# Kernel tuning notes

Measured on AMD Instinct MI355X. Metric: run time of the kernel, lower is better.

## Reference

```python
import jax, jax.numpy as jnp
import numpy as np

B, N = 16, 80
TEXT_DIM, AUDIO_DIM = 1024, 512
FD, FO = 512, 512          # bilinear pooling D, O
DH = 384                   # hidden_dim
L = 2                      # gnn_layers
NC = 7                     # num_class
IN_DIM = DH * (L + 1) + FO # out_mlp input dim


def _w(key, shape, scale=0.02):
    return (jax.random.normal(key, shape, dtype=jnp.float32) * scale)


def setup_inputs() -> dict:
    key = jax.random.key(0)
    ks = list(jax.random.split(key, 40))
    inp = {
        "features_text": jax.random.normal(ks[0], (B, N, TEXT_DIM), dtype=jnp.float32),
        "features_audio": jax.random.normal(ks[1], (B, N, AUDIO_DIM), dtype=jnp.float32),
        "adj": jnp.ones((B, N, N), dtype=jnp.int32),
        "s_mask": jax.random.randint(ks[2], (B, N, N), 0, 2, dtype=jnp.int32),
        "s_mask_onehot": jnp.zeros((B, N, N, 2), dtype=jnp.float32),
        "lengths": jnp.full((N and B,), N, dtype=jnp.int64) if False else jnp.full((B,), N, dtype=jnp.int32),
        # bilinear pooling
        "U1_w": _w(ks[3], (FD, TEXT_DIM)),
        "U2_w": _w(ks[4], (FD, AUDIO_DIM)),
        "P_w": _w(ks[5], (FO, FD)), "P_b": jnp.zeros((FO,), jnp.float32),
        "V1_w": _w(ks[6], (FO, TEXT_DIM)),
        "V2_w": _w(ks[7], (FO, AUDIO_DIM)),
        # fc1
        "fc1_w": _w(ks[8], (DH, FO)), "fc1_b": jnp.zeros((DH,), jnp.float32),
        # per-layer GAT (stacked on leading layer dim)
        "gat_w": _w(ks[9], (L, 1, 2 * DH)), "gat_b": jnp.zeros((L, 1), jnp.float32),
        "Wr0": _w(ks[10], (L, DH, DH)), "Wr1": _w(ks[11], (L, DH, DH)),
        # GRU cells (torch GRUCell layout: weight_ih (3H,H), weight_hh (3H,H))
        "gruC_wi": _w(ks[12], (L, 3 * DH, DH)), "gruC_wh": _w(ks[13], (L, 3 * DH, DH)),
        "gruC_bi": jnp.zeros((L, 3 * DH), jnp.float32), "gruC_bh": jnp.zeros((L, 3 * DH), jnp.float32),
        "gruP_wi": _w(ks[14], (L, 3 * DH, DH)), "gruP_wh": _w(ks[15], (L, 3 * DH, DH)),
        "gruP_bi": jnp.zeros((L, 3 * DH), jnp.float32), "gruP_bh": jnp.zeros((L, 3 * DH), jnp.float32),
        # out_mlp: Linear(in_dim,H) ReLU, Linear(H,H) ReLU, Linear(H,NC)
        "mlp_w0": _w(ks[16], (DH, IN_DIM)), "mlp_b0": jnp.zeros((DH,), jnp.float32),
        "mlp_w1": _w(ks[17], (DH, DH)), "mlp_b1": jnp.zeros((DH,), jnp.float32),
        "mlp_w2": _w(ks[18], (NC, DH)), "mlp_b2": jnp.zeros((NC,), jnp.float32),
    }
    return inp


def _gru_cell(x, h, wi, wh, bi, bh):
    gi = x @ wi.T + bi
    gh = h @ wh.T + bh
    i_r, i_z, i_n = jnp.split(gi, 3, axis=-1)
    h_r, h_z, h_n = jnp.split(gh, 3, axis=-1)
    r = jax.nn.sigmoid(i_r + h_r)
    z = jax.nn.sigmoid(i_z + h_z)
    n = jnp.tanh(i_n + r * h_n)
    return (1.0 - z) * n + z * h


def reference(features_text, features_audio, adj, s_mask, s_mask_onehot, lengths,
              U1_w, U2_w, P_w, P_b, V1_w, V2_w, fc1_w, fc1_b,
              gat_w, gat_b, Wr0, Wr1,
              gruC_wi, gruC_wh, gruC_bi, gruC_bh,
              gruP_wi, gruP_wh, gruP_bi, gruP_bh,
              mlp_w0, mlp_b0, mlp_w1, mlp_b1, mlp_w2, mlp_b2):
    # bilinear pooling fusion
    c_ = jax.nn.sigmoid(features_text @ U1_w.T) * jax.nn.sigmoid(features_audio @ U2_w.T)
    fused = c_ @ P_w.T + P_b + features_text @ V1_w.T + features_audio @ V2_w.T  # (B,N,FO)
    H0 = jax.nn.relu(fused @ fc1_w.T + fc1_b)                                    # (B,N,DH)

    n = H0.shape[1]
    adj_f = adj.astype(H0.dtype)
    s_f = s_mask.astype(H0.dtype)
    pos = jnp.arange(n)
    adj_t = jnp.swapaxes(adj_f, 0, 1)  # (N,B,N)
    s_t = jnp.swapaxes(s_f, 0, 1)      # (N,B,N)

    Hs = [H0]
    for l in range(gat_w.shape[0]):
        wq, wk = gat_w[l, 0, :H0.shape[2]], gat_w[l, 0, H0.shape[2]:]
        gb = gat_b[l, 0]
        wr0, wr1 = Wr0[l], Wr1[l]
        cwi, cwh, cbi, cbh = gruC_wi[l], gruC_wh[l], gruC_bi[l], gruC_bh[l]
        pwi, pwh, pbi, pbh = gruP_wi[l], gruP_wh[l], gruP_bi[l], gruP_bh[l]
        Hl = Hs[-1]

        def step(H1, xs):
            xi, adj_i, s_i, i = xs                              # xi (B,DH)
            # GAT_dialoggcn_v1 score: linear(cat(Q,K))
            alpha = (xi @ wq)[:, None] + H1 @ wk + gb           # (B,N)
            mask = adj_i * (pos < i).astype(alpha.dtype)        # only past, adj-allowed
            alpha = alpha - (1.0 - mask) * 1e30
            w = jax.nn.softmax(alpha, axis=-1)                  # (B,N)
            sm = s_i[..., None]
            V = (H1 @ wr0.T) * sm + (H1 @ wr1.T) * (1.0 - sm)   # (B,N,DH)
            M = jnp.einsum('bn,bnd->bd', w, V)
            M = jnp.where(i == 0, jnp.zeros_like(M), M)         # i=0: no attention, M=0
            C = _gru_cell(xi, M, cwi, cwh, cbi, cbh)
            P = _gru_cell(M, xi, pwi, pwh, pbi, pbh)
            Hnew = C + P
            H1 = jax.lax.dynamic_update_slice(H1, Hnew[:, None, :], (0, i, 0))
            return H1, Hnew

        xs = (jnp.swapaxes(Hl, 0, 1), adj_t, s_t, jnp.arange(n))
        _, ys = jax.lax.scan(step, jnp.zeros_like(Hl), xs)
        Hs.append(jnp.swapaxes(ys, 0, 1))

    Hcat = jnp.concatenate(Hs + [fused], axis=2)  # (B,N,IN_DIM)
    # attentive_node_features with nodal_att_type=None is identity; dropout eval = identity
    h = jax.nn.relu(Hcat @ mlp_w0.T + mlp_b0)
    h = jax.nn.relu(h @ mlp_w1.T + mlp_b1)
    logits = h @ mlp_w2.T + mlp_b2
    return jax.nn.log_softmax(logits, axis=2)
```

## Files before the change

kernel.cpp:

```cpp
#include <hip/hip_runtime.h>
#include <hip/hip_bf16.h>
#include <math.h>

#define BB 16
#define NN 80
#define DH_ 384
#define LDH 1664

typedef unsigned int uint;
typedef unsigned long long u64;

__global__ __launch_bounds__(256)
void gemm64(const float* __restrict__ A, int lda,
            const float* __restrict__ W, const float* __restrict__ Wb, int ldw,
            const float* __restrict__ bias,
            float* __restrict__ C, int ldc,
            int K, int act, int accum)
{
    __shared__ float As[16][68];
    __shared__ float Bs[16][68];
    const int tid = threadIdx.x;
    const int tx = tid & 15, ty = tid >> 4;
    const int r0 = blockIdx.y * 64, o0 = blockIdx.x * 64;

    float acc[4][4];
#pragma unroll
    for (int u = 0; u < 4; ++u)
#pragma unroll
        for (int v = 0; v < 4; ++v) acc[u][v] = 0.f;

    const int srow = tid >> 2;
    const int kq = (tid & 3) << 2;
    const float* asrc = A + (r0 + srow) * lda;
    const float* wsrc;
    {
        int orow = o0 + srow;
        wsrc = (Wb && orow >= 512) ? (Wb + (orow - 512) * ldw) : (W + orow * ldw);
    }

    for (int kb = 0; kb < K; kb += 16) {
        float4 va = *(const float4*)(asrc + kb + kq);
        float4 vb = *(const float4*)(wsrc + kb + kq);
        As[kq + 0][srow] = va.x; As[kq + 1][srow] = va.y;
        As[kq + 2][srow] = va.z; As[kq + 3][srow] = va.w;
        Bs[kq + 0][srow] = vb.x; Bs[kq + 1][srow] = vb.y;
        Bs[kq + 2][srow] = vb.z; Bs[kq + 3][srow] = vb.w;
        __syncthreads();
#pragma unroll
        for (int k = 0; k < 16; ++k) {
            float4 a = *(const float4*)&As[k][ty * 4];
            float4 bv = *(const float4*)&Bs[k][tx * 4];
            float av[4] = {a.x, a.y, a.z, a.w};
            float bb[4] = {bv.x, bv.y, bv.z, bv.w};
#pragma unroll
            for (int u = 0; u < 4; ++u)
#pragma unroll
                for (int v = 0; v < 4; ++v)
                    acc[u][v] = fmaf(av[u], bb[v], acc[u][v]);
        }
        __syncthreads();
    }
#pragma unroll
    for (int u = 0; u < 4; ++u) {
        int r = r0 + ty * 4 + u;
#pragma unroll
        for (int v = 0; v < 4; ++v) {
            int o = o0 + tx * 4 + v;
            float c = acc[u][v];
            if (bias) c += bias[o];
            if (accum) c += C[r * ldc + o];
            if (act == 1) c = fmaxf(c, 0.f);
            else if (act == 2) c = 1.f / (1.f + expf(-c));
            else if (act == 3 && o < 512) c = 1.f / (1.f + expf(-c));
            C[r * ldc + o] = c;
        }
    }
}

__global__ void ew2(const float* __restrict__ T1, const float* __restrict__ T2,
                    float* __restrict__ CBuf, float* __restrict__ Hc)
{
    int idx = blockIdx.x * 256 + threadIdx.x;
    int r = idx >> 9, c = idx & 511;
    CBuf[idx] = T1[r * 1024 + c] * T2[r * 1024 + c];
    Hc[r * LDH + 1152 + c] = T1[r * 1024 + 512 + c] + T2[r * 1024 + 512 + c];
}

__device__ __forceinline__ uint packbf(float lo, float hi)
{
    uint a = __float_as_uint(lo);
    a = (a + 0x7fffu + ((a >> 16) & 1u)) >> 16;
    uint b = __float_as_uint(hi);
    b = (b + 0x7fffu + ((b >> 16) & 1u)) & 0xffff0000u;
    return a | b;
}
__device__ __forceinline__ float bflo(uint u) { return __uint_as_float(u << 16); }
__device__ __forceinline__ float bfhi(uint u) { return __uint_as_float(u & 0xffff0000u); }

__global__ void trans_wg3(const float* __restrict__ cwh, const float* __restrict__ pwi,
                          uint* __restrict__ WgPk)
{
    int idx = blockIdx.x * 256 + threadIdx.x;
    int l = idx / 442368;
    int r = idx % 442368;
    int g = r / 27648;
    int r2 = r % 27648;
    int k = r2 / 72, cp = r2 % 72;
    float v[2];
#pragma unroll
    for (int u = 0; u < 2; ++u) {
        int c = 2 * cp + u;
        int idx6 = c / 24, o = c % 24, d = g * 24 + o;
        v[u] = (idx6 < 3) ? cwh[l * 442368 + (idx6 * 384 + d) * 384 + k]
                          : pwi[l * 442368 + ((idx6 - 3) * 384 + d) * 384 + k];
    }
    WgPk[idx] = packbf(v[0], v[1]);
}

__global__ void trans_wr3(const float* __restrict__ Wr0, const float* __restrict__ Wr1,
                          uint* __restrict__ WrPk)
{
    int idx = blockIdx.x * 256 + threadIdx.x;
    int l = idx / 147456;
    int r = idx % 147456;
    int g = r / 9216;
    int r2 = r % 9216;
    int k = r2 / 24, dl = r2 % 24;
    int row = g * 24 + dl;
    float w0 = Wr0[l * 147456 + row * 384 + k];
    float w1 = Wr1[l * 147456 + row * 384 + k];
    WrPk[idx] = packbf(w0, w1);
}

__global__ void gpre_prep(const float* __restrict__ cwi, const float* __restrict__ pwh,
                          const float* __restrict__ cbi, const float* __restrict__ pbh,
                          float* __restrict__ gw, float* __restrict__ gb_)
{
    int idx = blockIdx.x * 256 + threadIdx.x;
    int l = idx / 884736;
    int r = idx % 884736;
    int o = r / 384, k = r % 384;
    gw[idx] = (o < 1152) ? cwi[l * 442368 + o * 384 + k]
                         : pwh[l * 442368 + (o - 1152) * 384 + k];
    if (k == 0)
        gb_[l * 2304 + o] = (o < 1152) ? cbi[l * 1152 + o] : pbh[l * 1152 + o - 1152];
}

__global__ __launch_bounds__(256)
void qpre_k(const float* __restrict__ Hc, int hin, const float* __restrict__ wq,
            float* __restrict__ q)
{
    int wave = threadIdx.x >> 6, lane = threadIdx.x & 63;
    int row = blockIdx.x * 4 + wave;
    const float* hp = Hc + row * LDH + hin;
    float s = 0.f;
#pragma unroll
    for (int u = 0; u < 6; ++u) s = fmaf(hp[lane + 64 * u], wq[lane + 64 * u], s);
#pragma unroll
    for (int m = 1; m < 64; m <<= 1) s += __shfl_xor(s, m);
    if (lane == 0) q[row] = s;
}

#define ALD64(p)    __hip_atomic_load((p), __ATOMIC_RELAXED, __HIP_MEMORY_SCOPE_AGENT)
#define AST64(p, v) __hip_atomic_store((p), (v), __ATOMIC_RELAXED, __HIP_MEMORY_SCOPE_AGENT)

__global__ __launch_bounds__(512)
void scan10(float* Hc, int hin, int hout,
            const float* __restrict__ gPre,
            const uint* __restrict__ WrPkl,
            const uint* __restrict__ WgPkl,
            const float* __restrict__ qpre,
            const float* __restrict__ gatwl,
            const float* __restrict__ gatbl,
            const int* __restrict__ adj,
            const int* __restrict__ smask,
            const float* __restrict__ cbh,
            const float* __restrict__ pbi,
            u64* __restrict__ X1,
            u64* __restrict__ X2)
{
    const int wg = blockIdx.x;
    const int b = wg >> 4, g = wg & 15;
    const int t = threadIdx.x;

    extern __shared__ uint WgL[];
    __shared__ uint WrL[384 * 25];
    __shared__ uint Pc16[NN][25];
    __shared__ float kvS[NN];
    __shared__ float2 ws01[NN];
    __shared__ float Mv[DH_];
    __shared__ float uA[864];
    __shared__ float gs[144];
    __shared__ float karr[16];

    {
        const uint* src = WgPkl + g * 27648;
        for (int idx = t; idx < 27648; idx += 512) WgL[idx] = src[idx];
        const uint* src2 = WrPkl + g * 9216;
        for (int idx = t; idx < 9216; idx += 512) {
            int k = idx / 24, dl = idx % 24;
            WrL[k * 25 + dl] = src2[idx];
        }
    }
    __syncthreads();

    u64* X1b = X1 + b * 1024;
    u64* X2b = X2 + b * 512;
    const float gb = gatbl[0];

    int ca0 = 0, cs0 = 0, ca1 = 0, cs1 = 0;
    float cq = 0.f;
    int na0 = 0, ns0 = 0, na1 = 0, ns1 = 0;
    float nq = 0.f;

    float gpv = 0.f, xv = 0.f;

    for (int i = 0; i < NN; ++i) {
        const int rowi = b * NN + i;

        if (t < 144) gpv = gPre[rowi * 2304 + (t / 24) * 384 + g * 24 + (t % 24)];
        else if (t < 168) xv = Hc[rowi * LDH + hin + g * 24 + (t - 144)];
        if (t < 64) {
            int ip = (i + 1 < NN) ? (i + 1) : (NN - 1);
            int rp = b * NN + ip;
            na0 = adj[rp * NN + t];
            ns0 = smask[rp * NN + t];
            if (t + 64 < NN) { na1 = adj[rp * NN + t + 64]; ns1 = smask[rp * NN + t + 64]; }
            nq = qpre[rp];
        }
        __syncthreads();

        if (i > 0) {
            const u64* Xs2 = X2b + ((i - 1) & 1) * 256;
            if (t < 256) {
                int gg = t >> 4, j = t & 15;
                if (j < 13) {
                    u64 w;
                    do { w = ALD64(&Xs2[gg * 16 + j]); } while ((uint)(w >> 32) != (uint)i);
                    uint lo = (uint)w;
                    if (j < 12) {
                        uA[gg * 24 + 2 * j]     = bflo(lo);
                        uA[gg * 24 + 2 * j + 1] = bfhi(lo);
                    } else {
                        karr[gg] = __uint_as_float(lo);
                    }
                }
            }
            __syncthreads();

            if (t == 400) {
                float s = 0.f;
#pragma unroll
                for (int u = 0; u < 16; ++u) s += karr[u];
                kvS[i - 1] = s;
            }
            if (t < 384) {
                int dl0 = t >> 4, sub = t & 15, part = sub & 7, half = sub >> 3;
                float acc = 0.f;
#pragma unroll 8
                for (int m = 0; m < 48; ++m) {
                    int k = part + 8 * m;
                    uint u = WrL[k * 25 + dl0];
                    float w2_ = half ? bfhi(u) : bflo(u);
                    acc = fmaf(w2_, uA[k], acc);
                }
                acc += __shfl_xor(acc, 1);
                acc += __shfl_xor(acc, 2);
                acc += __shfl_xor(acc, 4);
                float other = __shfl_xor(acc, 8);
                if (sub == 0) Pc16[i - 1][dl0] = packbf(acc, other);
            }
            __syncthreads();

            if (t < 64) {
                float q = cq + gb;
                int j0 = t, j1 = t + 64;
                float a0v = -1e30f, a1v = -1e30f;
                if (j0 < i && ca0 != 0) a0v = q + kvS[j0];
                if (j1 < i && ca1 != 0) a1v = q + kvS[j1];
                float mx = fmaxf(a0v, a1v);
#pragma unroll
                for (int m = 1; m < 64; m <<= 1) mx = fmaxf(mx, __shfl_xor(mx, m));
                float e0 = expf(a0v - mx);
                float e1 = (j1 < NN) ? expf(a1v - mx) : 0.f;
                float ss = e0 + e1;
#pragma unroll
                for (int m = 1; m < 64; m <<= 1) ss += __shfl_xor(ss, m);
                float inv = 1.f / ss;
                float w0 = e0 * inv;
                float s0 = (float)cs0;
                ws01[j0] = make_float2(w0 * s0, w0 - w0 * s0);
                if (j1 < NN) {
                    float w1 = e1 * inv;
                    float s1 = (float)cs1;
                    ws01[j1] = make_float2(w1 * s1, w1 - w1 * s1);
                }
            }
            __syncthreads();

            u64* Xs1 = X1b + (i & 1) * 512;
            if (t < 384) {
                int dl0 = t >> 4, sub = t & 15;
                float acc = 0.f;
                for (int j = sub; j < i; j += 16) {
                    uint u = Pc16[j][dl0];
                    float2 w2_ = ws01[j];
                    acc = fmaf(w2_.x, bflo(u), acc);
                    acc = fmaf(w2_.y, bfhi(u), acc);
                }
                acc += __shfl_xor(acc, 1);
                acc += __shfl_xor(acc, 2);
                acc += __shfl_xor(acc, 4);
                acc += __shfl_xor(acc, 8);
                if (sub == 0)
                    AST64(&Xs1[g * 32 + dl0],
                          ((u64)(uint)(i + 1) << 32) | (u64)__float_as_uint(acc));
            }

            if (t < 512) {
                int gg = t >> 5, j = t & 31;
                if (j < 24) {
                    u64 wm;
                    do { wm = ALD64(&Xs1[gg * 32 + j]); } while ((uint)(wm >> 32) != (uint)(i + 1));
                    Mv[gg * 24 + j] = __uint_as_float((uint)wm);
                }
            }
            __syncthreads();
        } else {
            if (t < 384) Mv[t] = 0.f;
            __syncthreads();
        }

        if (t < 64) { ca0 = na0; cs0 = ns0; ca1 = na1; cs1 = ns1; cq = nq; }

        if (t < 432) {
            int cp = t % 72, kt = t / 72;
            int kbase = kt * 64;
            float a0 = 0.f, a1 = 0.f;
#pragma unroll 8
            for (int kk = 0; kk < 64; ++kk) {
                uint u = WgL[(kbase + kk) * 72 + cp];
                float m = Mv[kbase + kk];
                a0 = fmaf(bflo(u), m, a0);
                a1 = fmaf(bfhi(u), m, a1);
            }
            uA[kt * 144 + 2 * cp] = a0;
            uA[kt * 144 + 2 * cp + 1] = a1;
        }
        __syncthreads();
        if (t < 144) {
            float s = 0.f;
#pragma unroll
            for (int kt = 0; kt < 6; ++kt) s += uA[kt * 144 + t];
            gs[t] = s;
        }
        __syncthreads();

        if (t < 144) uA[t] = gpv;
        else if (t < 168) uA[t] = xv;
        __syncthreads();

        u64* Xs2w = X2b + (i & 1) * 256;
        if (t < 32) {
            float kp = 0.f, h = 0.f;
            if (t < 24) {
                int dg = g * 24 + t;
                float m = Mv[dg];
                float gir = uA[t], giz = uA[24 + t], gin = uA[48 + t];
                float ghr = gs[t] + cbh[dg];
                float ghz = gs[24 + t] + cbh[384 + dg];
                float ghn = gs[48 + t] + cbh[768 + dg];
                float r = 1.f / (1.f + expf(-(gir + ghr)));
                float z = 1.f / (1.f + expf(-(giz + ghz)));
                float n = tanhf(gin + r * ghn);
                float Cc = (1.f - z) * n + z * m;
                float pir = gs[72 + t] + pbi[dg];
                float piz = gs[96 + t] + pbi[384 + dg];
                float pin = gs[120 + t] + pbi[768 + dg];
                float phr = uA[72 + t], phz = uA[96 + t], phn = uA[120 + t];
                float r2 = 1.f / (1.f + expf(-(pir + phr)));
                float z2 = 1.f / (1.f + expf(-(piz + phz)));
                float n2 = tanhf(pin + r2 * phn);
                float x = uA[144 + t];
                float Pp = (1.f - z2) * n2 + z2 * x;
                h = Cc + Pp;
                Hc[rowi * LDH + hout + dg] = h;
                kp = h * gatwl[384 + dg];
            }
            int src = (t < 12) ? 2 * t : 0;
            float ha = __shfl(h, src);
            float hb = __shfl(h, src + 1);
            if (t < 12)
                AST64(&Xs2w[g * 16 + t],
                      ((u64)(uint)(i + 1) << 32) | (u64)packbf(ha, hb));
#pragma unroll
            for (int m = 16; m >= 1; m >>= 1) kp += __shfl_down(kp, m);
            if (t == 0)
                AST64(&Xs2w[g * 16 + 12],
                      ((u64)(uint)(i + 1) << 32) | (u64)__float_as_uint(kp));
        }
    }
}

__global__ __launch_bounds__(256)
void mlp_final(const float* __restrict__ h, const float* __restrict__ w2,
               const float* __restrict__ b2, float* __restrict__ out)
{
    int wave = threadIdx.x >> 6, lane = threadIdx.x & 63;
    int r = blockIdx.x * 4 + wave;
    float hreg[6];
#pragma unroll
    for (int m = 0; m < 6; ++m) hreg[m] = h[r * 384 + lane + 64 * m];
    float logit[7];
#pragma unroll
    for (int c = 0; c < 7; ++c) {
        float s = 0.f;
#pragma unroll
        for (int m = 0; m < 6; ++m)
            s = fmaf(hreg[m], w2[c * 384 + lane + 64 * m], s);
#pragma unroll
        for (int m = 1; m < 64; m <<= 1) s += __shfl_xor(s, m);
        logit[c] = s + b2[c];
    }
    float mx = logit[0];
#pragma unroll
    for (int c = 1; c < 7; ++c) mx = fmaxf(mx, logit[c]);
    float se = 0.f;
#pragma unroll
    for (int c = 0; c < 7; ++c) se += expf(logit[c] - mx);
    float lse = mx + logf(se);
    if (lane < 7) out[r * 7 + lane] = logit[lane] - lse;
}

extern "C" void kernel_launch(void* const* d_in, const int* in_sizes, int n_in,
                              void* d_out, int out_size, void* d_ws, size_t ws_size,
                              hipStream_t stream)
{
    const float* ftext = (const float*)d_in[0];
    const float* faud  = (const float*)d_in[1];
    const int*   adj   = (const int*)d_in[2];
    const int*   smask = (const int*)d_in[3];
    const float* U1    = (const float*)d_in[6];
    const float* U2    = (const float*)d_in[7];
    const float* Pw    = (const float*)d_in[8];
    const float* Pb    = (const float*)d_in[9];
    const float* V1    = (const float*)d_in[10];
    const float* V2    = (const float*)d_in[11];
    const float* fc1w  = (const float*)d_in[12];
    const float* fc1b  = (const float*)d_in[13];
    const float* gatw  = (const float*)d_in[14];
    const float* gatb  = (const float*)d_in[15];
    const float* Wr0   = (const float*)d_in[16];
    const float* Wr1   = (const float*)d_in[17];
    const float* cwi   = (const float*)d_in[18];
    const float* cwh   = (const float*)d_in[19];
    const float* cbi   = (const float*)d_in[20];
    const float* cbh   = (const float*)d_in[21];
    const float* pwi   = (const float*)d_in[22];
    const float* pwh   = (const float*)d_in[23];
    const float* pbi   = (const float*)d_in[24];
    const float* pbh   = (const float*)d_in[25];
    const float* w0    = (const float*)d_in[26];
    const float* b0    = (const float*)d_in[27];
    const float* w1    = (const float*)d_in[28];
    const float* b1    = (const float*)d_in[29];
    const float* w2    = (const float*)d_in[30];
    const float* b2    = (const float*)d_in[31];
    float* out = (float*)d_out;
    float* ws = (float*)d_ws;

    float* Hcat  = ws;
    float* gPre  = Hcat + 2129920;
    float* T1b   = gPre;
    float* T2b   = gPre + 1310720;
    float* CBuf  = gPre + 2949120;
    uint*  WgPk  = (uint*)(CBuf + 655360);
    uint*  WrPk  = WgPk + 884736;
    float* gw    = (float*)(WrPk + 294912);
    float* gb_   = gw + 1769472;
    float* qpreB = gb_ + 4608;
    u64*   X1l0  = (u64*)(qpreB + 2560);
    u64*   X2l0  = X1l0 + 16384;
    u64*   X1l1  = X2l0 + 8192;
    u64*   X2l1  = X1l1 + 16384;

    dim3 blk(256);
    auto gemm = [&](const float* A, int lda, const float* W, const float* Wb, int ldw,
                    const float* bias, float* C, int ldc, int K, int O,
                    int act, int accum) {
        dim3 grid(O / 64, 1280 / 64);
        gemm64<<<grid, blk, 0, stream>>>(A, lda, W, Wb, ldw, bias, C, ldc, K, act, accum);
    };

    hipMemsetAsync(X1l0, 0, (size_t)(16384 + 8192) * 2 * sizeof(u64), stream);

    trans_wg3<<<3456, 256, 0, stream>>>(cwh, pwi, WgPk);
    trans_wr3<<<1152, 256, 0, stream>>>(Wr0, Wr1, WrPk);
    gpre_prep<<<6912, 256, 0, stream>>>(cwi, pwh, cbi, pbh, gw, gb_);

    gemm(ftext, 1024, U1, V1, 1024, nullptr, T1b, 1024, 1024, 1024, 3, 0);
    gemm(faud,  512,  U2, V2, 512,  nullptr, T2b, 1024, 512,  1024, 3, 0);
    ew2<<<2560, 256, 0, stream>>>(T1b, T2b, CBuf, Hcat);
    gemm(CBuf, 512, Pw, nullptr, 512, Pb, Hcat + 1152, LDH, 512, 512, 0, 1);
    gemm(Hcat + 1152, LDH, fc1w, nullptr, 512, fc1b, Hcat, LDH, 512, 384, 1, 0);

    for (int l = 0; l < 2; ++l) {
        gemm(Hcat + l * 384, LDH, gw + l * 884736, nullptr, 384, gb_ + l * 2304,
             gPre, 2304, 384, 2304, 0, 0);
        qpre_k<<<320, 256, 0, stream>>>(Hcat, l * 384, gatw + l * 768, qpreB + l * 1280);
        scan10<<<256, 512, 110592, stream>>>(Hcat, l * 384, (l + 1) * 384, gPre,
                                             WrPk + l * 147456, WgPk + l * 442368,
                                             qpreB + l * 1280, gatw + l * 768, gatb + l,
                                             adj, smask, cbh + l * 1152, pbi + l * 1152,
                                             l ? X1l1 : X1l0, l ? X2l1 : X2l0);
    }

    gemm(Hcat, LDH, w0, nullptr, LDH, b0, CBuf, 384, 1664, 384, 1, 0);
    gemm(CBuf, 384, w1, nullptr, 384, b1, gPre, 384, 384, 384, 1, 0);
    mlp_final<<<320, 256, 0, stream>>>(gPre, w2, b2, out);
}
```

Before: 1.385 ms.

## Replace FP32 SIMT GEMMs with bf16 MFMA GEMM and pre-converted bf16 weights

Swaps the scalar FP32 64x64 tiled GEMM for a kernel that uses 16x16x32 bf16 MFMA instructions with XOR-swizzled LDS tiles. Activations are converted to bf16 on the fly, and all dense weights are converted once into a packed bf16 buffer by a single wcvt kernel, which also replaces gpre_prep. This moves the non-recurrent GEMMs onto matrix cores and halves weight traffic. The cost is bf16 rounding of inputs and weights, plus an extra conversion pass over all weights on every call.

New measurement: 1.153 ms, median of 2. 1.2x faster.

```diff
diff --git a/kernel.cpp b/kernel.cpp
--- a/kernel.cpp
+++ b/kernel.cpp
@@ -9,82 +9,8 @@
 
 typedef unsigned int uint;
 typedef unsigned long long u64;
-
-__global__ __launch_bounds__(256)
-void gemm64(const float* __restrict__ A, int lda,
-            const float* __restrict__ W, const float* __restrict__ Wb, int ldw,
-            const float* __restrict__ bias,
-            float* __restrict__ C, int ldc,
-            int K, int act, int accum)
-{
-    __shared__ float As[16][68];
-    __shared__ float Bs[16][68];
-    const int tid = threadIdx.x;
-    const int tx = tid & 15, ty = tid >> 4;
-    const int r0 = blockIdx.y * 64, o0 = blockIdx.x * 64;
-
-    float acc[4][4];
-#pragma unroll
-    for (int u = 0; u < 4; ++u)
-#pragma unroll
-        for (int v = 0; v < 4; ++v) acc[u][v] = 0.f;
-
-    const int srow = tid >> 2;
-    const int kq = (tid & 3) << 2;
-    const float* asrc = A + (r0 + srow) * lda;
-    const float* wsrc;
-    {
-        int orow = o0 + srow;
-        wsrc = (Wb && orow >= 512) ? (Wb + (orow - 512) * ldw) : (W + orow * ldw);
-    }
-
-    for (int kb = 0; kb < K; kb += 16) {
-        float4 va = *(const float4*)(asrc + kb + kq);
-        float4 vb = *(const float4*)(wsrc + kb + kq);
-        As[kq + 0][srow] = va.x; As[kq + 1][srow] = va.y;
-        As[kq + 2][srow] = va.z; As[kq + 3][srow] = va.w;
-        Bs[kq + 0][srow] = vb.x; Bs[kq + 1][srow] = vb.y;
-        Bs[kq + 2][srow] = vb.z; Bs[kq + 3][srow] = vb.w;
-        __syncthreads();
-#pragma unroll
-        for (int k = 0; k < 16; ++k) {
-            float4 a = *(const float4*)&As[k][ty * 4];
-            float4 bv = *(const float4*)&Bs[k][tx * 4];
-            float av[4] = {a.x, a.y, a.z, a.w};
-            float bb[4] = {bv.x, bv.y, bv.z, bv.w};
-#pragma unroll
-            for (int u = 0; u < 4; ++u)
-#pragma unroll
-                for (int v = 0; v < 4; ++v)
-                    acc[u][v] = fmaf(av[u], bb[v], acc[u][v]);
-        }
-        __syncthreads();
-    }
-#pragma unroll
-    for (int u = 0; u < 4; ++u) {
-        int r = r0 + ty * 4 + u;
-#pragma unroll
-        for (int v = 0; v < 4; ++v) {
-            int o = o0 + tx * 4 + v;
-            float c = acc[u][v];
-            if (bias) c += bias[o];
-            if (accum) c += C[r * ldc + o];
-            if (act == 1) c = fmaxf(c, 0.f);
-            else if (act == 2) c = 1.f / (1.f + expf(-c));
-            else if (act == 3 && o < 512) c = 1.f / (1.f + expf(-c));
-            C[r * ldc + o] = c;
-        }
-    }
-}
-
-__global__ void ew2(const float* __restrict__ T1, const float* __restrict__ T2,
-                    float* __restrict__ CBuf, float* __restrict__ Hc)
-{
-    int idx = blockIdx.x * 256 + threadIdx.x;
-    int r = idx >> 9, c = idx & 511;
-    CBuf[idx] = T1[r * 1024 + c] * T2[r * 1024 + c];
-    Hc[r * LDH + 1152 + c] = T1[r * 1024 + 512 + c] + T2[r * 1024 + 512 + c];
-}
+typedef __attribute__((ext_vector_type(8))) short short8;
+typedef __attribute__((ext_vector_type(4))) float f32x4;
 
 __device__ __forceinline__ uint packbf(float lo, float hi)
 {
@@ -96,6 +22,129 @@
 }
 __device__ __forceinline__ float bflo(uint u) { return __uint_as_float(u << 16); }
 __device__ __forceinline__ float bfhi(uint u) { return __uint_as_float(u & 0xffff0000u); }
+__device__ __forceinline__ unsigned short cvt1(float f)
+{
+    uint a = __float_as_uint(f);
+    return (unsigned short)((a + 0x7fffu + ((a >> 16) & 1u)) >> 16);
+}
+
+__global__ __launch_bounds__(256)
+void gemm_mfma(const float* __restrict__ A, int lda,
+               const unsigned short* __restrict__ W, int ldw,
+               const float* __restrict__ bias,
+               float* __restrict__ C, int ldc,
+               int K, int act, int accum)
+{
+    __shared__ __attribute__((aligned(16))) unsigned short As[4096];
+    __shared__ __attribute__((aligned(16))) unsigned short Bs[4096];
+    const int t = threadIdx.x;
+    const int lane = t & 63, wave = t >> 6;
+    const int r0 = blockIdx.y * 64, o0 = blockIdx.x * 64;
+
+    f32x4 acc0 = {0.f, 0.f, 0.f, 0.f};
+    f32x4 acc1 = acc0, acc2 = acc0, acc3 = acc0;
+
+    const int srow = t >> 2;
+    const int scp = (t & 3) * 2;
+    const int sw0 = ((scp ^ (srow & 7))) * 8;
+    const int sw1 = (((scp + 1) ^ (srow & 7))) * 8;
+    const float* ap0 = A + (size_t)(r0 + srow) * lda + scp * 8;
+    const unsigned short* bp0 = W + (size_t)(o0 + srow) * ldw + scp * 8;
+
+    const int fr = lane & 15, kg = lane >> 4;
+    const int fsw = fr & 7;
+    const int arow = (wave * 16 + fr) * 64;
+
+    for (int kb = 0; kb < K; kb += 64) {
+        float4 a0 = *(const float4*)(ap0 + kb);
+        float4 a1 = *(const float4*)(ap0 + kb + 4);
+        float4 a2 = *(const float4*)(ap0 + kb + 8);
+        float4 a3 = *(const float4*)(ap0 + kb + 12);
+        uint4 b0 = *(const uint4*)(bp0 + kb);
+        uint4 b1 = *(const uint4*)(bp0 + kb + 8);
+        uint4 apk0, apk1;
+        apk0.x = packbf(a0.x, a0.y); apk0.y = packbf(a0.z, a0.w);
+        apk0.z = packbf(a1.x, a1.y); apk0.w = packbf(a1.z, a1.w);
+        apk1.x = packbf(a2.x, a2.y); apk1.y = packbf(a2.z, a2.w);
+        apk1.z = packbf(a3.x, a3.y); apk1.w = packbf(a3.z, a3.w);
+        *(uint4*)&As[srow * 64 + sw0] = apk0;
+        *(uint4*)&As[srow * 64 + sw1] = apk1;
+        *(uint4*)&Bs[srow * 64 + sw0] = b0;
+        *(uint4*)&Bs[srow * 64 + sw1] = b1;
+        __syncthreads();
+#pragma unroll
+        for (int h = 0; h < 2; ++h) {
+            int ach = kg + 4 * h;
+            short8 af = *(const short8*)&As[arow + ((ach ^ fsw)) * 8];
+            short8 bf0 = *(const short8*)&Bs[(0 * 16 + fr) * 64 + ((ach ^ fsw)) * 8];
+            short8 bf1 = *(const short8*)&Bs[(1 * 16 + fr) * 64 + ((ach ^ fsw)) * 8];
+            short8 bf2 = *(const short8*)&Bs[(2 * 16 + fr) * 64 + ((ach ^ fsw)) * 8];
+            short8 bf3 = *(const short8*)&Bs[(3 * 16 + fr) * 64 + ((ach ^ fsw)) * 8];
+            acc0 = __builtin_amdgcn_mfma_f32_16x16x32_bf16(af, bf0, acc0, 0, 0, 0);
+            acc1 = __builtin_amdgcn_mfma_f32_16x16x32_bf16(af, bf1, acc1, 0, 0, 0);
+            acc2 = __builtin_amdgcn_mfma_f32_16x16x32_bf16(af, bf2, acc2, 0, 0, 0);
+            acc3 = __builtin_amdgcn_mfma_f32_16x16x32_bf16(af, bf3, acc3, 0, 0, 0);
+        }
+        __syncthreads();
+    }
+    const int rg = lane >> 4;
+    f32x4 av[4] = {acc0, acc1, acc2, acc3};
+#pragma unroll
+    for (int c = 0; c < 4; ++c) {
+        int col = o0 + c * 16 + fr;
+        float bv = bias ? bias[col] : 0.f;
+#pragma unroll
+        for (int r = 0; r < 4; ++r) {
+            int row = r0 + wave * 16 + rg * 4 + r;
+            float v = av[c][r] + bv;
+            if (accum) v += C[(size_t)row * ldc + col];
+            if (act == 1) v = fmaxf(v, 0.f);
+            else if (act == 2) v = 1.f / (1.f + expf(-v));
+            else if (act == 3 && col < 512) v = 1.f / (1.f + expf(-v));
+            C[(size_t)row * ldc + col] = v;
+        }
+    }
+}
+
+__global__ void wcvt(const float* __restrict__ U1, const float* __restrict__ V1,
+                     const float* __restrict__ U2, const float* __restrict__ V2,
+                     const float* __restrict__ Pw, const float* __restrict__ fc1w,
+                     const float* __restrict__ cwi, const float* __restrict__ pwh,
+                     const float* __restrict__ w0, const float* __restrict__ w1,
+                     const float* __restrict__ cbi, const float* __restrict__ pbh,
+                     unsigned short* __restrict__ wB, float* __restrict__ gb_)
+{
+    int idx = blockIdx.x * 256 + threadIdx.x;
+    if (idx < 4587520) {
+        float v;
+        if      (idx < 524288)  v = U1[idx];
+        else if (idx < 1048576) v = V1[idx - 524288];
+        else if (idx < 1310720) v = U2[idx - 1048576];
+        else if (idx < 1572864) v = V2[idx - 1310720];
+        else if (idx < 1835008) v = Pw[idx - 1572864];
+        else if (idx < 2031616) v = fc1w[idx - 1835008];
+        else if (idx < 2473984) v = cwi[idx - 2031616];
+        else if (idx < 2916352) v = pwh[idx - 2473984];
+        else if (idx < 3358720) v = cwi[442368 + idx - 2916352];
+        else if (idx < 3801088) v = pwh[442368 + idx - 3358720];
+        else if (idx < 4440064) v = w0[idx - 3801088];
+        else                    v = w1[idx - 4440064];
+        wB[idx] = cvt1(v);
+    } else if (idx < 4592128) {
+        int j = idx - 4587520;
+        int l = j / 2304, o = j % 2304;
+        gb_[j] = (o < 1152) ? cbi[l * 1152 + o] : pbh[l * 1152 + o - 1152];
+    }
+}
+
+__global__ void ew2(const float* __restrict__ T1, const float* __restrict__ T2,
+                    float* __restrict__ CBuf, float* __restrict__ Hc)
+{
+    int idx = blockIdx.x * 256 + threadIdx.x;
+    int r = idx >> 9, c = idx & 511;
+    CBuf[idx] = T1[r * 1024 + c] * T2[r * 1024 + c];
+    Hc[r * LDH + 1152 + c] = T1[r * 1024 + 512 + c] + T2[r * 1024 + 512 + c];
+}
 
 __global__ void trans_wg3(const float* __restrict__ cwh, const float* __restrict__ pwi,
                           uint* __restrict__ WgPk)
@@ -130,20 +179,6 @@
     float w0 = Wr0[l * 147456 + row * 384 + k];
     float w1 = Wr1[l * 147456 + row * 384 + k];
     WrPk[idx] = packbf(w0, w1);
-}
-
-__global__ void gpre_prep(const float* __restrict__ cwi, const float* __restrict__ pwh,
-                          const float* __restrict__ cbi, const float* __restrict__ pbh,
-                          float* __restrict__ gw, float* __restrict__ gb_)
-{
-    int idx = blockIdx.x * 256 + threadIdx.x;
-    int l = idx / 884736;
-    int r = idx % 884736;
-    int o = r / 384, k = r % 384;
-    gw[idx] = (o < 1152) ? cwi[l * 442368 + o * 384 + k]
-                         : pwh[l * 442368 + (o - 1152) * 384 + k];
-    if (k == 0)
-        gb_[l * 2304 + o] = (o < 1152) ? cbi[l * 1152 + o] : pbh[l * 1152 + o - 1152];
 }
 
 __global__ __launch_bounds__(256)
@@ -212,7 +247,6 @@
     float cq = 0.f;
     int na0 = 0, ns0 = 0, na1 = 0, ns1 = 0;
     float nq = 0.f;
-
     float gpv = 0.f, xv = 0.f;
 
     for (int i = 0; i < NN; ++i) {
@@ -470,43 +504,44 @@
     float* ws = (float*)d_ws;
 
     float* Hcat  = ws;
-    float* gPre  = Hcat + 2129920;
+    float* gPre  = ws + 2129920;
     float* T1b   = gPre;
     float* T2b   = gPre + 1310720;
-    float* CBuf  = gPre + 2949120;
-    uint*  WgPk  = (uint*)(CBuf + 655360);
-    uint*  WrPk  = WgPk + 884736;
-    float* gw    = (float*)(WrPk + 294912);
-    float* gb_   = gw + 1769472;
-    float* qpreB = gb_ + 4608;
-    u64*   X1l0  = (u64*)(qpreB + 2560);
+    float* CBuf  = ws + 5079040;
+    uint*  WgPk  = (uint*)(ws + 5734400);
+    uint*  WrPk  = (uint*)(ws + 6619136);
+    float* gb_   = ws + 6914048;
+    float* qpreB = ws + 6918656;
+    u64*   X1l0  = (u64*)(ws + 6921216);
     u64*   X2l0  = X1l0 + 16384;
     u64*   X1l1  = X2l0 + 8192;
     u64*   X2l1  = X1l1 + 16384;
-
-    dim3 blk(256);
-    auto gemm = [&](const float* A, int lda, const float* W, const float* Wb, int ldw,
-                    const float* bias, float* C, int ldc, int K, int O,
-                    int act, int accum) {
-        dim3 grid(O / 64, 1280 / 64);
-        gemm64<<<grid, blk, 0, stream>>>(A, lda, W, Wb, ldw, bias, C, ldc, K, act, accum);
+    unsigned short* wB = (unsigned short*)(ws + 7019520);
+
+    auto g = [&](const float* A, int lda, size_t woff, int ldw,
+                 const float* bias, float* C, int ldc, int K, int N,
+                 int act, int accum) {
+        dim3 grid(N / 64, 1280 / 64);
+        gemm_mfma<<<grid, 256, 0, stream>>>(A, lda, wB + woff, ldw, bias, C, ldc,
+                                            K, act, accum);
     };
 
     hipMemsetAsync(X1l0, 0, (size_t)(16384 + 8192) * 2 * sizeof(u64), stream);
 
+    wcvt<<<17938, 256, 0, stream>>>(U1, V1, U2, V2, Pw, fc1w, cwi, pwh, w0, w1,
+                                    cbi, pbh, wB, gb_);
     trans_wg3<<<3456, 256, 0, stream>>>(cwh, pwi, WgPk);
     trans_wr3<<<1152, 256, 0, stream>>>(Wr0, Wr1, WrPk);
-    gpre_prep<<<6912, 256, 0, stream>>>(cwi, pwh, cbi, pbh, gw, gb_);
-
-    gemm(ftext, 1024, U1, V1, 1024, nullptr, T1b, 1024, 1024, 1024, 3, 0);
-    gemm(faud,  512,  U2, V2, 512,  nullptr, T2b, 1024, 512,  1024, 3, 0);
+
+    g(ftext, 1024, 0, 1024, nullptr, T1b, 1024, 1024, 1024, 3, 0);
+    g(faud, 512, 1048576, 512, nullptr, T2b, 1024, 512, 1024, 3, 0);
     ew2<<<2560, 256, 0, stream>>>(T1b, T2b, CBuf, Hcat);
-    gemm(CBuf, 512, Pw, nullptr, 512, Pb, Hcat + 1152, LDH, 512, 512, 0, 1);
-    gemm(Hcat + 1152, LDH, fc1w, nullptr, 512, fc1b, Hcat, LDH, 512, 384, 1, 0);
+    g(CBuf, 512, 1572864, 512, Pb, Hcat + 1152, LDH, 512, 512, 0, 1);
+    g(Hcat + 1152, LDH, 1835008, 512, fc1b, Hcat, LDH, 512, 384, 1, 0);
 
     for (int l = 0; l < 2; ++l) {
-        gemm(Hcat + l * 384, LDH, gw + l * 884736, nullptr, 384, gb_ + l * 2304,
-             gPre, 2304, 384, 2304, 0, 0);
+        g(Hcat + l * 384, LDH, 2031616 + (size_t)l * 884736, 384,
+          gb_ + l * 2304, gPre, 2304, 384, 2304, 0, 0);
         qpre_k<<<320, 256, 0, stream>>>(Hcat, l * 384, gatw + l * 768, qpreB + l * 1280);
         scan10<<<256, 512, 110592, stream>>>(Hcat, l * 384, (l + 1) * 384, gPre,
                                              WrPk + l * 147456, WgPk + l * 442368,
@@ -515,7 +550,7 @@
                                              l ? X1l1 : X1l0, l ? X2l1 : X2l0);
     }
 
-    gemm(Hcat, LDH, w0, nullptr, LDH, b0, CBuf, 384, 1664, 384, 1, 0);
-    gemm(CBuf, 384, w1, nullptr, 384, b1, gPre, 384, 384, 384, 1, 0);
+    g(Hcat, LDH, 3801088, 1664, b0, CBuf, 384, 1664, 384, 1, 0);
+    g(CBuf, 384, 4440064, 384, b1, gPre, 384, 384, 384, 1, 0);
     mlp_final<<<320, 256, 0, stream>>>(gPre, w2, b2, out);
 }
```
